# Optimization experiments

Hardware: AMD Instinct MI355X
Metric: run time of the kernel (lower is better)

## Reference

```python
import jax, jax.numpy as jnp
import numpy as np


def setup_inputs() -> dict:
    key = jax.random.key(0)
    k_x, k_w1, k_w2 = jax.random.split(key, 3)
    b, d, m, h = 256, 2048, 64, 128  # batch, d_model, history_length, d_out
    lim1 = 1.0 / np.sqrt(m + h)
    lim2 = 1.0 / np.sqrt(h + d)
    x = jax.random.normal(k_x, (b, d, m), dtype=jnp.float32)
    w1 = jax.random.uniform(k_w1, (m, h, d), dtype=jnp.float32, minval=-lim1, maxval=lim1)
    b1 = jnp.zeros((1, h, d), dtype=jnp.float32)
    w2 = jax.random.uniform(k_w2, (h, d), dtype=jnp.float32, minval=-lim2, maxval=lim2)
    b2 = jnp.zeros((1, h), dtype=jnp.float32)
    return {"x": x, "w1": w1, "b1": b1, "w2": w2, "b2": b2}


def reference(x, w1, b1, w2, b2):
    # per-neuron (per-d) MLP: contract over history m, then over hidden h
    hidden = jnp.einsum('bdm,mhd->bhd', x, w1) + b1  # (b, h, d)
    out = jnp.einsum('bhd,hd->bh', hidden, w2) + b2  # (b, h)
    return out
```

## Files before the change

### kernel.cpp

```cpp
#include <hip/hip_runtime.h>

typedef unsigned short u16;
typedef __attribute__((ext_vector_type(8))) short short8;
typedef __attribute__((ext_vector_type(4))) float f32x4;

#define D_TOT 2048
#define M_TOT 64
#define H_TOT 128
#define B_TOT 256
#define NG    256
#define XB    131072
#define W1M   262144

__device__ __forceinline__ u16 f2bf(float f) {
  unsigned u = __builtin_bit_cast(unsigned, f);
  u = (u + 0x7fffu + ((u >> 16) & 1u)) >> 16;
  return (u16)u;
}
__device__ __forceinline__ float bf2f(u16 v) {
  unsigned u = ((unsigned)v) << 16;
  return __builtin_bit_cast(float, u);
}

__global__ __launch_bounds__(256)
void nlm_p0(const float* __restrict__ b1, const float* __restrict__ w2,
            const float* __restrict__ b2, float* __restrict__ ch) {
  const int h = blockIdx.x, t = threadIdx.x;
  const float4* pb = (const float4*)(b1 + (size_t)h * D_TOT);
  const float4* pw = (const float4*)(w2 + (size_t)h * D_TOT);
  float s = 0.f;
  for (int i = t; i < D_TOT / 4; i += 256) {
    float4 a = pb[i], w = pw[i];
    s += a.x * w.x + a.y * w.y + a.z * w.z + a.w * w.w;
  }
  __shared__ float red[256];
  red[t] = s;
  __syncthreads();
  for (int off = 128; off > 0; off >>= 1) {
    if (t < off) red[t] += red[t + off];
    __syncthreads();
  }
  if (t == 0) ch[h] = red[0] + b2[h];
}

__global__ __launch_bounds__(512, 4)
void nlm_p1(const float* __restrict__ x, const float* __restrict__ w1,
            const float* __restrict__ w2, u16* __restrict__ partial) {
  __shared__ __align__(16) u16 As[128 * 72];
  __shared__ __align__(16) u16 Bs[128 * 72];

  const int tid  = threadIdx.x;
  const int grp  = blockIdx.x & 63;
  const int jj   = blockIdx.x >> 6;
  const int g    = grp * 4 + (jj & 3);
  const int bh   = jj >> 2;
  const int d0   = g * 8;
  const int lane = tid & 63, wave = tid >> 6;
  const int wm   = wave >> 2;
  const int wn   = wave & 3;
  const int quad = lane >> 4, l16 = lane & 15;

  const int a_b  = tid >> 2;
  const int a_r  = tid & 3;
  const int a_m4 = a_r >> 1;
  const int a_j  = (a_r & 1) * 4;
  const float* xbase = x + (size_t)(bh * 128 + a_b) * XB
                         + (size_t)(d0 + a_j) * M_TOT + a_m4 * 4;

  const int b_h   = tid & 127;
  const int b_ml0 = tid >> 7;
  const float* w2p = w2 + (size_t)b_h * D_TOT + d0;
  const float4 s0 = *(const float4*)(w2p);
  const float4 s1 = *(const float4*)(w2p + 4);

  f32x4 acc[4][2];
#pragma unroll
  for (int i = 0; i < 4; ++i)
#pragma unroll
    for (int j = 0; j < 2; ++j) acc[i][j] = (f32x4){0.f, 0.f, 0.f, 0.f};

  for (int c = 0; c < 8; ++c) {
    {
      const float* xp = xbase + c * 8;
      float4 v0 = *(const float4*)(xp);
      float4 v1 = *(const float4*)(xp + M_TOT);
      float4 v2 = *(const float4*)(xp + 2 * M_TOT);
      float4 v3 = *(const float4*)(xp + 3 * M_TOT);
      u16* ap = As + a_b * 72 + a_m4 * 32 + a_j;
      *(ushort4*)(ap)      = make_ushort4(f2bf(v0.x), f2bf(v1.x), f2bf(v2.x), f2bf(v3.x));
      *(ushort4*)(ap + 8)  = make_ushort4(f2bf(v0.y), f2bf(v1.y), f2bf(v2.y), f2bf(v3.y));
      *(ushort4*)(ap + 16) = make_ushort4(f2bf(v0.z), f2bf(v1.z), f2bf(v2.z), f2bf(v3.z));
      *(ushort4*)(ap + 24) = make_ushort4(f2bf(v0.w), f2bf(v1.w), f2bf(v2.w), f2bf(v3.w));
    }
#pragma unroll
    for (int i = 0; i < 2; ++i) {
      const int ml = b_ml0 + i * 4;
      const float* w1p = w1 + (size_t)(c * 8 + ml) * W1M + (size_t)b_h * D_TOT + d0;
      float4 a0 = *(const float4*)(w1p);
      float4 a1 = *(const float4*)(w1p + 4);
      u16* bp = Bs + b_h * 72 + ml * 8;
      *(ushort4*)(bp)     = make_ushort4(f2bf(a0.x * s0.x), f2bf(a0.y * s0.y),
                                         f2bf(a0.z * s0.z), f2bf(a0.w * s0.w));
      *(ushort4*)(bp + 4) = make_ushort4(f2bf(a1.x * s1.x), f2bf(a1.y * s1.y),
                                         f2bf(a1.z * s1.z), f2bf(a1.w * s1.w));
    }
    __syncthreads();
#pragma unroll
    for (int s = 0; s < 2; ++s) {
      short8 af[4], bq[2];
#pragma unroll
      for (int i = 0; i < 4; ++i)
        af[i] = *(const short8*)(As + (wm * 64 + i * 16 + l16) * 72 + s * 32 + quad * 8);
#pragma unroll
      for (int j = 0; j < 2; ++j)
        bq[j] = *(const short8*)(Bs + (wn * 32 + j * 16 + l16) * 72 + s * 32 + quad * 8);
#pragma unroll
      for (int i = 0; i < 4; ++i)
#pragma unroll
        for (int j = 0; j < 2; ++j)
          acc[i][j] = __builtin_amdgcn_mfma_f32_16x16x32_bf16(af[i], bq[j], acc[i][j], 0, 0, 0);
    }
    __syncthreads();
  }

#pragma unroll
  for (int i = 0; i < 4; ++i)
#pragma unroll
    for (int j = 0; j < 2; ++j) {
      const int hcol = wn * 32 + j * 16 + l16;
#pragma unroll
      for (int r = 0; r < 4; ++r) {
        const int brow = bh * 128 + wm * 64 + i * 16 + quad * 4 + r;
        __builtin_nontemporal_store(
            f2bf(acc[i][j][r]),
            partial + ((size_t)brow * NG + g) * H_TOT + hcol);
      }
    }
}

__global__ __launch_bounds__(256)
void nlm_p2(const u16* __restrict__ partial, const float* __restrict__ ch,
            float* __restrict__ out) {
  const int b = blockIdx.x, t = threadIdx.x;
  const int h2   = t & 63;
  const int half = t >> 6;
  const u16* base = partial + ((size_t)b * NG + half * 64) * H_TOT + 2 * h2;
  float s0 = 0.f, s1 = 0.f;
#pragma unroll 8
  for (int gg = 0; gg < 64; ++gg) {
    unsigned v = __builtin_nontemporal_load((const unsigned*)(base + (size_t)gg * H_TOT));
    s0 += bf2f((u16)(v & 0xffffu));
    s1 += bf2f((u16)(v >> 16));
  }
  __shared__ float red0[256], red1[256];
  red0[t] = s0;
  red1[t] = s1;
  __syncthreads();
  if (t < 64) {
    float a0 = red0[t] + red0[t + 64] + red0[t + 128] + red0[t + 192];
    float a1 = red1[t] + red1[t + 64] + red1[t + 128] + red1[t + 192];
    out[(size_t)b * H_TOT + 2 * t]     = a0 + ch[2 * t];
    out[(size_t)b * H_TOT + 2 * t + 1] = a1 + ch[2 * t + 1];
  }
}

extern "C" void kernel_launch(void* const* d_in, const int* in_sizes, int n_in,
                              void* d_out, int out_size, void* d_ws, size_t ws_size,
                              hipStream_t stream) {
  const float* x  = (const float*)d_in[0];
  const float* w1 = (const float*)d_in[1];
  const float* b1 = (const float*)d_in[2];
  const float* w2 = (const float*)d_in[3];
  const float* b2 = (const float*)d_in[4];
  float* out = (float*)d_out;

  u16*   partial = (u16*)d_ws;
  float* ch      = (float*)((char*)d_ws + (size_t)B_TOT * NG * H_TOT * sizeof(u16));

  nlm_p0<<<dim3(128), dim3(256), 0, stream>>>(b1, w2, b2, ch);
  nlm_p1<<<dim3(512), dim3(512), 0, stream>>>(x, w1, w2, partial);
  nlm_p2<<<dim3(256), dim3(256), 0, stream>>>(partial, ch, out);
}
```

Baseline: 308.6 us.

## Prepack scaled bf16 weights in a separate kernel and halve batch tile

Adds a preprocessing kernel that multiplies w1 by w2, converts to bf16, and stores it in a layout matching the main kernel's B tile, so the GEMM kernel loads contiguous bf16 rows instead of strided fp32 w1 with conversion. The main kernel now uses 64-row batch tiles over 1024 blocks, which doubles the number of times the packed weights are read, and loads x contiguously along m. The packed weight tensor needs extra workspace and an extra launch, and the partial stores are no longer nontemporal.

```diff
diff --git a/kernel.cpp b/kernel.cpp
--- a/kernel.cpp
+++ b/kernel.cpp
@@ -43,97 +43,114 @@
   if (t == 0) ch[h] = red[0] + b2[h];
 }
 
+__global__ __launch_bounds__(256)
+void nlm_pw(const float* __restrict__ w1, const float* __restrict__ w2,
+            u16* __restrict__ Bp) {
+  const int gq  = blockIdx.x & 63;
+  const int hb  = blockIdx.x >> 6;
+  const int dq0 = gq * 32;
+  const int t   = threadIdx.x;
+  __shared__ u16 tile[32 * 16 * 64];
+
+#pragma unroll
+  for (int rep = 0; rep < 4; ++rep) {
+    const int tau = rep * 256 + t;
+    const int h_l = tau >> 6, m = tau & 63;
+    const int h   = hb * 16 + h_l;
+    const float* w1p = w1 + (size_t)m * W1M + (size_t)h * D_TOT + dq0;
+    const float* w2p = w2 + (size_t)h * D_TOT + dq0;
+    u16* dst = tile + h_l * 64 + m;
+#pragma unroll
+    for (int q = 0; q < 8; ++q) {
+      float4 a = *(const float4*)(w1p + q * 4);
+      float4 s = *(const float4*)(w2p + q * 4);
+      dst[(q * 4 + 0) * 1024] = f2bf(a.x * s.x);
+      dst[(q * 4 + 1) * 1024] = f2bf(a.y * s.y);
+      dst[(q * 4 + 2) * 1024] = f2bf(a.z * s.z);
+      dst[(q * 4 + 3) * 1024] = f2bf(a.w * s.w);
+    }
+  }
+  __syncthreads();
+#pragma unroll 4
+  for (int dc = 0; dc < 32; ++dc) {
+    const int g = gq * 4 + (dc >> 3), c = dc & 7;
+    u16* out = Bp + (((size_t)g * 8 + c) * H_TOT + hb * 16) * 64 + t * 4;
+    *(ushort4*)out = *(const ushort4*)(tile + dc * 1024 + t * 4);
+  }
+}
+
 __global__ __launch_bounds__(512, 4)
-void nlm_p1(const float* __restrict__ x, const float* __restrict__ w1,
-            const float* __restrict__ w2, u16* __restrict__ partial) {
-  __shared__ __align__(16) u16 As[128 * 72];
+void nlm_p1(const float* __restrict__ x, const u16* __restrict__ Bp,
+            u16* __restrict__ partial) {
+  __shared__ __align__(16) u16 As[64 * 72];
   __shared__ __align__(16) u16 Bs[128 * 72];
 
   const int tid  = threadIdx.x;
-  const int grp  = blockIdx.x & 63;
-  const int jj   = blockIdx.x >> 6;
-  const int g    = grp * 4 + (jj & 3);
-  const int bh   = jj >> 2;
+  const int g    = blockIdx.x & 255;
+  const int bq   = blockIdx.x >> 8;
   const int d0   = g * 8;
   const int lane = tid & 63, wave = tid >> 6;
   const int wm   = wave >> 2;
   const int wn   = wave & 3;
   const int quad = lane >> 4, l16 = lane & 15;
 
-  const int a_b  = tid >> 2;
-  const int a_r  = tid & 3;
-  const int a_m4 = a_r >> 1;
-  const int a_j  = (a_r & 1) * 4;
-  const float* xbase = x + (size_t)(bh * 128 + a_b) * XB
-                         + (size_t)(d0 + a_j) * M_TOT + a_m4 * 4;
-
-  const int b_h   = tid & 127;
-  const int b_ml0 = tid >> 7;
-  const float* w2p = w2 + (size_t)b_h * D_TOT + d0;
-  const float4 s0 = *(const float4*)(w2p);
-  const float4 s1 = *(const float4*)(w2p + 4);
-
-  f32x4 acc[4][2];
-#pragma unroll
-  for (int i = 0; i < 4; ++i)
+  const int a_bl = tid >> 3, a_p = tid & 7;
+  const float* xrow = x + (size_t)(bq * 64 + a_bl) * XB
+                        + (size_t)d0 * M_TOT + a_p * 8;
+  const int b_h = tid >> 2, b_qp = tid & 3;
+  const u16* bsrc = Bp + ((size_t)g * 8 * H_TOT + b_h) * 64 + b_qp * 16;
+
+  f32x4 acc[2][2];
+#pragma unroll
+  for (int i = 0; i < 2; ++i)
 #pragma unroll
     for (int j = 0; j < 2; ++j) acc[i][j] = (f32x4){0.f, 0.f, 0.f, 0.f};
 
   for (int c = 0; c < 8; ++c) {
     {
-      const float* xp = xbase + c * 8;
+      const float* xp = xrow + c * M_TOT;
       float4 v0 = *(const float4*)(xp);
-      float4 v1 = *(const float4*)(xp + M_TOT);
-      float4 v2 = *(const float4*)(xp + 2 * M_TOT);
-      float4 v3 = *(const float4*)(xp + 3 * M_TOT);
-      u16* ap = As + a_b * 72 + a_m4 * 32 + a_j;
-      *(ushort4*)(ap)      = make_ushort4(f2bf(v0.x), f2bf(v1.x), f2bf(v2.x), f2bf(v3.x));
-      *(ushort4*)(ap + 8)  = make_ushort4(f2bf(v0.y), f2bf(v1.y), f2bf(v2.y), f2bf(v3.y));
-      *(ushort4*)(ap + 16) = make_ushort4(f2bf(v0.z), f2bf(v1.z), f2bf(v2.z), f2bf(v3.z));
-      *(ushort4*)(ap + 24) = make_ushort4(f2bf(v0.w), f2bf(v1.w), f2bf(v2.w), f2bf(v3.w));
-    }
-#pragma unroll
-    for (int i = 0; i < 2; ++i) {
-      const int ml = b_ml0 + i * 4;
-      const float* w1p = w1 + (size_t)(c * 8 + ml) * W1M + (size_t)b_h * D_TOT + d0;
-      float4 a0 = *(const float4*)(w1p);
-      float4 a1 = *(const float4*)(w1p + 4);
-      u16* bp = Bs + b_h * 72 + ml * 8;
-      *(ushort4*)(bp)     = make_ushort4(f2bf(a0.x * s0.x), f2bf(a0.y * s0.y),
-                                         f2bf(a0.z * s0.z), f2bf(a0.w * s0.w));
-      *(ushort4*)(bp + 4) = make_ushort4(f2bf(a1.x * s1.x), f2bf(a1.y * s1.y),
-                                         f2bf(a1.z * s1.z), f2bf(a1.w * s1.w));
+      float4 v1 = *(const float4*)(xp + 4);
+      short8 av;
+      av[0] = (short)f2bf(v0.x); av[1] = (short)f2bf(v0.y);
+      av[2] = (short)f2bf(v0.z); av[3] = (short)f2bf(v0.w);
+      av[4] = (short)f2bf(v1.x); av[5] = (short)f2bf(v1.y);
+      av[6] = (short)f2bf(v1.z); av[7] = (short)f2bf(v1.w);
+      *(short8*)(As + a_bl * 72 + a_p * 8) = av;
+    }
+    {
+      const u16* bp = bsrc + (size_t)c * (H_TOT * 64);
+      *(short8*)(Bs + b_h * 72 + b_qp * 16)     = *(const short8*)(bp);
+      *(short8*)(Bs + b_h * 72 + b_qp * 16 + 8) = *(const short8*)(bp + 8);
     }
     __syncthreads();
 #pragma unroll
     for (int s = 0; s < 2; ++s) {
-      short8 af[4], bq[2];
-#pragma unroll
-      for (int i = 0; i < 4; ++i)
-        af[i] = *(const short8*)(As + (wm * 64 + i * 16 + l16) * 72 + s * 32 + quad * 8);
+      short8 af[2], bf[2];
+#pragma unroll
+      for (int i = 0; i < 2; ++i)
+        af[i] = *(const short8*)(As + (wm * 32 + i * 16 + l16) * 72 + s * 32 + quad * 8);
 #pragma unroll
       for (int j = 0; j < 2; ++j)
-        bq[j] = *(const short8*)(Bs + (wn * 32 + j * 16 + l16) * 72 + s * 32 + quad * 8);
-#pragma unroll
-      for (int i = 0; i < 4; ++i)
+        bf[j] = *(const short8*)(Bs + (wn * 32 + j * 16 + l16) * 72 + s * 32 + quad * 8);
+#pragma unroll
+      for (int i = 0; i < 2; ++i)
 #pragma unroll
         for (int j = 0; j < 2; ++j)
-          acc[i][j] = __builtin_amdgcn_mfma_f32_16x16x32_bf16(af[i], bq[j], acc[i][j], 0, 0, 0);
+          acc[i][j] = __builtin_amdgcn_mfma_f32_16x16x32_bf16(af[i], bf[j], acc[i][j], 0, 0, 0);
     }
     __syncthreads();
   }
 
 #pragma unroll
-  for (int i = 0; i < 4; ++i)
+  for (int i = 0; i < 2; ++i)
 #pragma unroll
     for (int j = 0; j < 2; ++j) {
       const int hcol = wn * 32 + j * 16 + l16;
 #pragma unroll
       for (int r = 0; r < 4; ++r) {
-        const int brow = bh * 128 + wm * 64 + i * 16 + quad * 4 + r;
-        __builtin_nontemporal_store(
-            f2bf(acc[i][j][r]),
-            partial + ((size_t)brow * NG + g) * H_TOT + hcol);
+        const int brow = bq * 64 + wm * 32 + i * 16 + quad * 4 + r;
+        partial[((size_t)brow * NG + g) * H_TOT + hcol] = f2bf(acc[i][j][r]);
       }
     }
 }
@@ -175,9 +192,12 @@
   float* out = (float*)d_out;
 
   u16*   partial = (u16*)d_ws;
-  float* ch      = (float*)((char*)d_ws + (size_t)B_TOT * NG * H_TOT * sizeof(u16));
-
-  nlm_p0<<<dim3(128), dim3(256), 0, stream>>>(b1, w2, b2, ch);
-  nlm_p1<<<dim3(512), dim3(512), 0, stream>>>(x, w1, w2, partial);
-  nlm_p2<<<dim3(256), dim3(256), 0, stream>>>(partial, ch, out);
-}
+  u16*   Bp      = (u16*)((char*)d_ws + (size_t)B_TOT * NG * H_TOT * sizeof(u16));
+  float* ch      = (float*)((char*)d_ws + (size_t)B_TOT * NG * H_TOT * sizeof(u16)
+                                        + (size_t)NG * 8 * H_TOT * 64 * sizeof(u16));
+
+  nlm_p0<<<dim3(128),  dim3(256), 0, stream>>>(b1, w2, b2, ch);
+  nlm_pw<<<dim3(512),  dim3(256), 0, stream>>>(w1, w2, Bp);
+  nlm_p1<<<dim3(1024), dim3(512), 0, stream>>>(x, Bp, partial);
+  nlm_p2<<<dim3(256),  dim3(256), 0, stream>>>(partial, ch, out);
+}
```

Result: faster. 266.8 us (-13.5%).
